# Optimization experiments

Hardware: AMD Instinct MI355X
Metric: run time of the kernel (lower is better)

Reference implementation:

```python
import jax, jax.numpy as jnp
import numpy as np

HEAD_DIM = 32
KERNEL = 9
DILATION = 3


def setup_inputs() -> dict:
    key = jax.random.key(0)
    k1, k2, k3 = jax.random.split(key, 3)
    B, d, L = 4, 512, 4096
    q = jax.random.normal(k1, (B, d, 1, L), dtype=jnp.float32)
    k = jax.random.normal(k2, (B, d, 1, L), dtype=jnp.float32)
    v = jax.random.normal(k3, (B, d, 1, L), dtype=jnp.float32)
    return {"q": q, "k": k, "v": v}


def reference(q, k, v):
    # q,k,v: [B, d, 1, L]; output: [B, 1, L, d]
    B, d, _, N = q.shape
    hd = HEAD_DIM
    h = d // hd
    K = KERNEL
    dil = DILATION
    pad = dil * (K - 1) // 2
    scale = hd ** -0.5

    # Window gather indices replicating nn.Unfold with zero padding.
    idx = jnp.arange(N)[:, None] + jnp.arange(K)[None, :] * dil - pad  # [N, K]
    valid = ((idx >= 0) & (idx < N)).astype(q.dtype)                   # [N, K]
    idxc = jnp.clip(idx, 0, N - 1)

    qr = q.reshape(B, h, hd, N)
    kr = k.reshape(B, h, hd, N)
    vr = v.reshape(B, h, hd, N)

    # Unfolded windows: [B, h, hd, N, K], zero outside bounds (like Unfold padding)
    kw = kr[:, :, :, idxc] * valid
    vw = vr[:, :, :, idxc] * valid

    attn = jnp.einsum('bhdn,bhdnk->bhnk', qr, kw) * scale
    attn = jax.nn.softmax(attn, axis=-1)
    out = jnp.einsum('bhnk,bhdnk->bhnd', attn, vw)  # [B, h, N, hd]
    # torch: transpose(1,2).reshape(B,1,N,d) -> heads concatenated per token
    return out.transpose(0, 2, 1, 3).reshape(B, 1, N, d)
```

## Files before the change

kernel.cpp:

```cpp
#include <hip/hip_runtime.h>
#include <math.h>

#define NPOS 4096
#define DCH  512
#define HD   32
#define NH   16
#define KW   9
#define DIL  3
#define PAD  12
#define TILE   128
#define NTILES (NPOS / TILE)
#define SPANT  (TILE + 2*PAD)
#define ROWF4  (SPANT / 4)
#define SLDS   156
#define CSPL   8
#define CPT    (HD / CSPL)
#define TPT    4
#define WSPAN  28

__global__ __launch_bounds__(256) void dilate_attn_kernel(
    const float* __restrict__ q,
    const float* __restrict__ k,
    const float* __restrict__ v,
    float* __restrict__ out)
{
    __shared__ float ks[HD * SLDS];
    __shared__ float vs[HD * SLDS];

    const int bh   = blockIdx.x >> 5;
    const int tile = blockIdx.x & (NTILES - 1);
    const int n0t  = tile * TILE;
    const int ws   = n0t - PAD;

    const size_t cb = (size_t)bh * HD * NPOS;
    const float* kg = k + cb;
    const float* vg = v + cb;
    const float* qg = q + cb;

    const bool easy = (ws >= 0) && (ws + SPANT <= NPOS);
    for (int p = threadIdx.x; p < HD * ROWF4; p += 256) {
        int row = p / ROWF4;
        int c4  = p - row * ROWF4;
        int g0  = ws + c4 * 4;
        const float* kr = kg + (size_t)row * NPOS;
        const float* vr = vg + (size_t)row * NPOS;
        float4 kk, vv;
        if (easy || (g0 >= 0 && g0 + 4 <= NPOS)) {
            kk = *(const float4*)(kr + g0);
            vv = *(const float4*)(vr + g0);
        } else {
            int i0 = min(max(g0 + 0, 0), NPOS - 1);
            int i1 = min(max(g0 + 1, 0), NPOS - 1);
            int i2 = min(max(g0 + 2, 0), NPOS - 1);
            int i3 = min(max(g0 + 3, 0), NPOS - 1);
            kk = make_float4(kr[i0], kr[i1], kr[i2], kr[i3]);
            vv = make_float4(vr[i0], vr[i1], vr[i2], vr[i3]);
        }
        *(float4*)&ks[row * SLDS + c4 * 4] = kk;
        *(float4*)&vs[row * SLDS + c4 * 4] = vv;
    }

    const int cs = threadIdx.x & (CSPL - 1);
    const int lg = threadIdx.x >> 3;
    const int n0 = n0t + lg * TPT;

    float4 qv[CPT];
#pragma unroll
    for (int i = 0; i < CPT; ++i) {
        int ch = cs * CPT + i;
        qv[i] = *(const float4*)(qg + (size_t)ch * NPOS + n0);
    }

    __syncthreads();

    float s[TPT][KW];
#pragma unroll
    for (int t = 0; t < TPT; ++t)
#pragma unroll
        for (int j = 0; j < KW; ++j) s[t][j] = 0.0f;

#pragma unroll
    for (int i = 0; i < CPT; ++i) {
        int row = cs * CPT + i;
        const float4* wp = (const float4*)&ks[row * SLDS + lg * TPT];
        float w[WSPAN];
#pragma unroll
        for (int u = 0; u < WSPAN / 4; ++u) {
            float4 x = wp[u];
            w[4*u] = x.x; w[4*u+1] = x.y; w[4*u+2] = x.z; w[4*u+3] = x.w;
        }
        float qt[TPT] = {qv[i].x, qv[i].y, qv[i].z, qv[i].w};
#pragma unroll
        for (int t = 0; t < TPT; ++t)
#pragma unroll
            for (int j = 0; j < KW; ++j)
                s[t][j] = fmaf(qt[t], w[t + 3*j], s[t][j]);
    }

#pragma unroll
    for (int t = 0; t < TPT; ++t)
#pragma unroll
        for (int j = 0; j < KW; ++j) {
            float x = s[t][j];
            x += __shfl_xor(x, 1);
            x += __shfl_xor(x, 2);
            x += __shfl_xor(x, 4);
            s[t][j] = x;
        }

    const float scale = 0.17677669529663687f;
#pragma unroll
    for (int t = 0; t < TPT; ++t) {
        float m = -INFINITY;
#pragma unroll
        for (int j = 0; j < KW; ++j) {
            float valid = ((unsigned)(n0 + t + 3*j - PAD) < NPOS) ? 1.0f : 0.0f;
            float x = s[t][j] * scale * valid;
            s[t][j] = x;
            m = fmaxf(m, x);
        }
        float sum = 0.0f;
#pragma unroll
        for (int j = 0; j < KW; ++j) {
            float e = __expf(s[t][j] - m);
            s[t][j] = e;
            sum += e;
        }
        float inv = 1.0f / sum;
#pragma unroll
        for (int j = 0; j < KW; ++j) {
            float valid = ((unsigned)(n0 + t + 3*j - PAD) < NPOS) ? 1.0f : 0.0f;
            s[t][j] *= inv * valid;
        }
    }

    float o[TPT][CPT];
#pragma unroll
    for (int t = 0; t < TPT; ++t)
#pragma unroll
        for (int i = 0; i < CPT; ++i) o[t][i] = 0.0f;

#pragma unroll
    for (int i = 0; i < CPT; ++i) {
        int row = cs * CPT + i;
        const float4* wp = (const float4*)&vs[row * SLDS + lg * TPT];
        float w[WSPAN];
#pragma unroll
        for (int u = 0; u < WSPAN / 4; ++u) {
            float4 x = wp[u];
            w[4*u] = x.x; w[4*u+1] = x.y; w[4*u+2] = x.z; w[4*u+3] = x.w;
        }
#pragma unroll
        for (int t = 0; t < TPT; ++t)
#pragma unroll
            for (int j = 0; j < KW; ++j)
                o[t][i] = fmaf(s[t][j], w[t + 3*j], o[t][i]);
    }

    const int b  = bh >> 4;
    const int hh = bh & (NH - 1);
#pragma unroll
    for (int t = 0; t < TPT; ++t) {
        float* op = out + ((size_t)(b * NPOS + n0 + t)) * DCH + hh * HD + cs * CPT;
        *(float4*)op = make_float4(o[t][0], o[t][1], o[t][2], o[t][3]);
    }
}

extern "C" void kernel_launch(void* const* d_in, const int* in_sizes, int n_in,
                              void* d_out, int out_size, void* d_ws, size_t ws_size,
                              hipStream_t stream) {
    const float* q = (const float*)d_in[0];
    const float* k = (const float*)d_in[1];
    const float* v = (const float*)d_in[2];
    float* out = (float*)d_out;

    const int grid = 4 * NH * NTILES;
    hipLaunchKernelGGL(dilate_attn_kernel, dim3(grid), dim3(256), 0, stream,
                       q, k, v, out);
}
```

Baseline: 147.8 us.

## Process four tiles per block with register-staged double-buffered LDS prefetch

Each block now handles four consecutive sequence tiles instead of one. The next tile's K/V/Q loads are issued into registers before the current tile's compute, then written into the alternate LDS buffer. This overlaps global-memory latency with compute and amortizes block setup. In exchange the grid shrinks by four to 512 blocks, LDS use doubles, and register pressure rises, which may lower occupancy and latency hiding on a memory-bound kernel.

```diff
diff --git a/kernel.cpp b/kernel.cpp
--- a/kernel.cpp
+++ b/kernel.cpp
@@ -17,6 +17,8 @@
 #define CPT    (HD / CSPL)
 #define TPT    4
 #define WSPAN  28
+#define NT4    4
+#define NLD    5
 
 __global__ __launch_bounds__(256) void dilate_attn_kernel(
     const float* __restrict__ q,
@@ -24,145 +26,185 @@
     const float* __restrict__ v,
     float* __restrict__ out)
 {
-    __shared__ float ks[HD * SLDS];
-    __shared__ float vs[HD * SLDS];
-
-    const int bh   = blockIdx.x >> 5;
-    const int tile = blockIdx.x & (NTILES - 1);
-    const int n0t  = tile * TILE;
-    const int ws   = n0t - PAD;
+    __shared__ float ks[2][HD * SLDS];
+    __shared__ float vs[2][HD * SLDS];
+
+    const int tid   = threadIdx.x;
+    const int tseq0 = blockIdx.x * NT4;
+    const int bh    = tseq0 >> 5;
+    const int tile0 = tseq0 & (NTILES - 1);
 
     const size_t cb = (size_t)bh * HD * NPOS;
     const float* kg = k + cb;
     const float* vg = v + cb;
     const float* qg = q + cb;
 
-    const bool easy = (ws >= 0) && (ws + SPANT <= NPOS);
-    for (int p = threadIdx.x; p < HD * ROWF4; p += 256) {
-        int row = p / ROWF4;
-        int c4  = p - row * ROWF4;
-        int g0  = ws + c4 * 4;
-        const float* kr = kg + (size_t)row * NPOS;
-        const float* vr = vg + (size_t)row * NPOS;
-        float4 kk, vv;
-        if (easy || (g0 >= 0 && g0 + 4 <= NPOS)) {
-            kk = *(const float4*)(kr + g0);
-            vv = *(const float4*)(vr + g0);
-        } else {
-            int i0 = min(max(g0 + 0, 0), NPOS - 1);
-            int i1 = min(max(g0 + 1, 0), NPOS - 1);
-            int i2 = min(max(g0 + 2, 0), NPOS - 1);
-            int i3 = min(max(g0 + 3, 0), NPOS - 1);
-            kk = make_float4(kr[i0], kr[i1], kr[i2], kr[i3]);
-            vv = make_float4(vr[i0], vr[i1], vr[i2], vr[i3]);
-        }
-        *(float4*)&ks[row * SLDS + c4 * 4] = kk;
-        *(float4*)&vs[row * SLDS + c4 * 4] = vv;
+    int  srow[NLD], scol[NLD];
+    bool sact[NLD];
+#pragma unroll
+    for (int u = 0; u < NLD; ++u) {
+        int p = tid + u * 256;
+        sact[u] = (p < HD * ROWF4);
+        int pp = sact[u] ? p : 0;
+        srow[u] = pp / ROWF4;
+        scol[u] = (pp - srow[u] * ROWF4) * 4;
     }
 
-    const int cs = threadIdx.x & (CSPL - 1);
-    const int lg = threadIdx.x >> 3;
-    const int n0 = n0t + lg * TPT;
+    const int cs = tid & (CSPL - 1);
+    const int lg = tid >> 3;
+
+    auto load_tile = [&](int tl, float4* kr, float4* vr, float4* qn) {
+        const int ws = tl * TILE - PAD;
+        const bool easy = (tl > 0) && (tl < NTILES - 1);
+#pragma unroll
+        for (int u = 0; u < NLD; ++u) {
+            if (!sact[u]) continue;
+            int g0 = ws + scol[u];
+            const float* krow = kg + (size_t)srow[u] * NPOS;
+            const float* vrow = vg + (size_t)srow[u] * NPOS;
+            if (easy || (g0 >= 0 && g0 + 4 <= NPOS)) {
+                kr[u] = *(const float4*)(krow + g0);
+                vr[u] = *(const float4*)(vrow + g0);
+            } else {
+                int i0 = min(max(g0 + 0, 0), NPOS - 1);
+                int i1 = min(max(g0 + 1, 0), NPOS - 1);
+                int i2 = min(max(g0 + 2, 0), NPOS - 1);
+                int i3 = min(max(g0 + 3, 0), NPOS - 1);
+                kr[u] = make_float4(krow[i0], krow[i1], krow[i2], krow[i3]);
+                vr[u] = make_float4(vrow[i0], vrow[i1], vrow[i2], vrow[i3]);
+            }
+        }
+        int n0 = tl * TILE + lg * TPT;
+#pragma unroll
+        for (int i = 0; i < CPT; ++i)
+            qn[i] = *(const float4*)(qg + (size_t)(cs * CPT + i) * NPOS + n0);
+    };
+
+    auto write_lds = [&](int buf, const float4* kr, const float4* vr) {
+#pragma unroll
+        for (int u = 0; u < NLD; ++u) {
+            if (!sact[u]) continue;
+            *(float4*)&ks[buf][srow[u] * SLDS + scol[u]] = kr[u];
+            *(float4*)&vs[buf][srow[u] * SLDS + scol[u]] = vr[u];
+        }
+    };
 
     float4 qv[CPT];
-#pragma unroll
-    for (int i = 0; i < CPT; ++i) {
-        int ch = cs * CPT + i;
-        qv[i] = *(const float4*)(qg + (size_t)ch * NPOS + n0);
+    {
+        float4 ka[NLD], va[NLD];
+        load_tile(tile0, ka, va, qv);
+        write_lds(0, ka, va);
     }
-
     __syncthreads();
 
-    float s[TPT][KW];
-#pragma unroll
-    for (int t = 0; t < TPT; ++t)
-#pragma unroll
-        for (int j = 0; j < KW; ++j) s[t][j] = 0.0f;
-
-#pragma unroll
-    for (int i = 0; i < CPT; ++i) {
-        int row = cs * CPT + i;
-        const float4* wp = (const float4*)&ks[row * SLDS + lg * TPT];
-        float w[WSPAN];
-#pragma unroll
-        for (int u = 0; u < WSPAN / 4; ++u) {
-            float4 x = wp[u];
-            w[4*u] = x.x; w[4*u+1] = x.y; w[4*u+2] = x.z; w[4*u+3] = x.w;
-        }
-        float qt[TPT] = {qv[i].x, qv[i].y, qv[i].z, qv[i].w};
-#pragma unroll
-        for (int t = 0; t < TPT; ++t)
-#pragma unroll
-            for (int j = 0; j < KW; ++j)
-                s[t][j] = fmaf(qt[t], w[t + 3*j], s[t][j]);
-    }
-
-#pragma unroll
-    for (int t = 0; t < TPT; ++t)
-#pragma unroll
-        for (int j = 0; j < KW; ++j) {
-            float x = s[t][j];
-            x += __shfl_xor(x, 1);
-            x += __shfl_xor(x, 2);
-            x += __shfl_xor(x, 4);
-            s[t][j] = x;
-        }
-
     const float scale = 0.17677669529663687f;
-#pragma unroll
-    for (int t = 0; t < TPT; ++t) {
-        float m = -INFINITY;
-#pragma unroll
-        for (int j = 0; j < KW; ++j) {
-            float valid = ((unsigned)(n0 + t + 3*j - PAD) < NPOS) ? 1.0f : 0.0f;
-            float x = s[t][j] * scale * valid;
-            s[t][j] = x;
-            m = fmaxf(m, x);
-        }
-        float sum = 0.0f;
-#pragma unroll
-        for (int j = 0; j < KW; ++j) {
-            float e = __expf(s[t][j] - m);
-            s[t][j] = e;
-            sum += e;
-        }
-        float inv = 1.0f / sum;
-#pragma unroll
-        for (int j = 0; j < KW; ++j) {
-            float valid = ((unsigned)(n0 + t + 3*j - PAD) < NPOS) ? 1.0f : 0.0f;
-            s[t][j] *= inv * valid;
-        }
-    }
-
-    float o[TPT][CPT];
-#pragma unroll
-    for (int t = 0; t < TPT; ++t)
-#pragma unroll
-        for (int i = 0; i < CPT; ++i) o[t][i] = 0.0f;
-
-#pragma unroll
-    for (int i = 0; i < CPT; ++i) {
-        int row = cs * CPT + i;
-        const float4* wp = (const float4*)&vs[row * SLDS + lg * TPT];
-        float w[WSPAN];
-#pragma unroll
-        for (int u = 0; u < WSPAN / 4; ++u) {
-            float4 x = wp[u];
-            w[4*u] = x.x; w[4*u+1] = x.y; w[4*u+2] = x.z; w[4*u+3] = x.w;
-        }
-#pragma unroll
-        for (int t = 0; t < TPT; ++t)
-#pragma unroll
-            for (int j = 0; j < KW; ++j)
-                o[t][i] = fmaf(s[t][j], w[t + 3*j], o[t][i]);
-    }
-
     const int b  = bh >> 4;
     const int hh = bh & (NH - 1);
-#pragma unroll
-    for (int t = 0; t < TPT; ++t) {
-        float* op = out + ((size_t)(b * NPOS + n0 + t)) * DCH + hh * HD + cs * CPT;
-        *(float4*)op = make_float4(o[t][0], o[t][1], o[t][2], o[t][3]);
+
+#pragma unroll 1
+    for (int it = 0; it < NT4; ++it) {
+        const int cur = it & 1;
+        const int tl  = tile0 + it;
+        const int n0  = tl * TILE + lg * TPT;
+
+        float4 kn[NLD], vn[NLD], qn[CPT];
+        if (it + 1 < NT4) load_tile(tl + 1, kn, vn, qn);
+
+        float s[TPT][KW];
+#pragma unroll
+        for (int t = 0; t < TPT; ++t)
+#pragma unroll
+            for (int j = 0; j < KW; ++j) s[t][j] = 0.0f;
+
+#pragma unroll
+        for (int i = 0; i < CPT; ++i) {
+            int row = cs * CPT + i;
+            const float4* wp = (const float4*)&ks[cur][row * SLDS + lg * TPT];
+            float w[WSPAN];
+#pragma unroll
+            for (int u = 0; u < WSPAN / 4; ++u) {
+                float4 x = wp[u];
+                w[4*u] = x.x; w[4*u+1] = x.y; w[4*u+2] = x.z; w[4*u+3] = x.w;
+            }
+            float qt[TPT] = {qv[i].x, qv[i].y, qv[i].z, qv[i].w};
+#pragma unroll
+            for (int t = 0; t < TPT; ++t)
+#pragma unroll
+                for (int j = 0; j < KW; ++j)
+                    s[t][j] = fmaf(qt[t], w[t + 3*j], s[t][j]);
+        }
+
+#pragma unroll
+        for (int t = 0; t < TPT; ++t)
+#pragma unroll
+            for (int j = 0; j < KW; ++j) {
+                float x = s[t][j];
+                x += __shfl_xor(x, 1);
+                x += __shfl_xor(x, 2);
+                x += __shfl_xor(x, 4);
+                s[t][j] = x;
+            }
+
+#pragma unroll
+        for (int t = 0; t < TPT; ++t) {
+            float m = -INFINITY;
+#pragma unroll
+            for (int j = 0; j < KW; ++j) {
+                float valid = ((unsigned)(n0 + t + 3*j - PAD) < NPOS) ? 1.0f : 0.0f;
+                float x = s[t][j] * scale * valid;
+                s[t][j] = x;
+                m = fmaxf(m, x);
+            }
+            float sum = 0.0f;
+#pragma unroll
+            for (int j = 0; j < KW; ++j) {
+                float e = __expf(s[t][j] - m);
+                s[t][j] = e;
+                sum += e;
+            }
+            float inv = 1.0f / sum;
+#pragma unroll
+            for (int j = 0; j < KW; ++j) {
+                float valid = ((unsigned)(n0 + t + 3*j - PAD) < NPOS) ? 1.0f : 0.0f;
+                s[t][j] *= inv * valid;
+            }
+        }
+
+        float o[TPT][CPT];
+#pragma unroll
+        for (int t = 0; t < TPT; ++t)
+#pragma unroll
+            for (int i = 0; i < CPT; ++i) o[t][i] = 0.0f;
+
+#pragma unroll
+        for (int i = 0; i < CPT; ++i) {
+            int row = cs * CPT + i;
+            const float4* wp = (const float4*)&vs[cur][row * SLDS + lg * TPT];
+            float w[WSPAN];
+#pragma unroll
+            for (int u = 0; u < WSPAN / 4; ++u) {
+                float4 x = wp[u];
+                w[4*u] = x.x; w[4*u+1] = x.y; w[4*u+2] = x.z; w[4*u+3] = x.w;
+            }
+#pragma unroll
+            for (int t = 0; t < TPT; ++t)
+#pragma unroll
+                for (int j = 0; j < KW; ++j)
+                    o[t][i] = fmaf(s[t][j], w[t + 3*j], o[t][i]);
+        }
+
+#pragma unroll
+        for (int t = 0; t < TPT; ++t) {
+            float* op = out + ((size_t)(b * NPOS + n0 + t)) * DCH + hh * HD + cs * CPT;
+            *(float4*)op = make_float4(o[t][0], o[t][1], o[t][2], o[t][3]);
+        }
+
+        if (it + 1 < NT4) {
+            write_lds(cur ^ 1, kn, vn);
+#pragma unroll
+            for (int i = 0; i < CPT; ++i) qv[i] = qn[i];
+        }
+        __syncthreads();
     }
 }
 
@@ -174,7 +216,7 @@
     const float* v = (const float*)d_in[2];
     float* out = (float*)d_out;
 
-    const int grid = 4 * NH * NTILES;
+    const int grid = 4 * NH * NTILES / NT4;
     hipLaunchKernelGGL(dilate_attn_kernel, dim3(grid), dim3(256), 0, stream,
                        q, k, v, out);
 }
```

Result: slower. 154.5 us (+4.5%).
